# Performance work log

Measured on AMD Instinct MI355X. Metric: run time of the kernel, lower is better.

## Reference

```python
import jax, jax.numpy as jnp
import numpy as np

EMBED = 384
HEADS = 6
HEAD_SIZE = EMBED // HEADS
EPS = 1e-5


def _layernorm(x, g, b):
    mu = jnp.mean(x, axis=-1, keepdims=True)
    var = jnp.mean(jnp.square(x - mu), axis=-1, keepdims=True)
    return (x - mu) * jax.lax.rsqrt(var + EPS) * g + b


def setup_inputs() -> dict:
    key = jax.random.key(0)
    ks = jax.random.split(key, 16)
    B, T = 64, 256
    s_in = 1.0 / np.sqrt(EMBED)
    return {
        "x": jax.random.normal(ks[0], (B, T, EMBED), dtype=jnp.float32),
        # per-head q/k/v projections, stacked over heads: [H, C, D]
        "Wq": jax.random.normal(ks[1], (HEADS, EMBED, HEAD_SIZE), dtype=jnp.float32) * s_in,
        "bq": jnp.zeros((HEADS, HEAD_SIZE), dtype=jnp.float32),
        "Wk": jax.random.normal(ks[2], (HEADS, EMBED, HEAD_SIZE), dtype=jnp.float32) * s_in,
        "bk": jnp.zeros((HEADS, HEAD_SIZE), dtype=jnp.float32),
        "Wv": jax.random.normal(ks[3], (HEADS, EMBED, HEAD_SIZE), dtype=jnp.float32) * s_in,
        "bv": jnp.zeros((HEADS, HEAD_SIZE), dtype=jnp.float32),
        "Wp": jax.random.normal(ks[4], (EMBED, EMBED), dtype=jnp.float32) * s_in,
        "bp": jnp.zeros((EMBED,), dtype=jnp.float32),
        "W1": jax.random.normal(ks[5], (EMBED, EMBED), dtype=jnp.float32) * s_in,
        "b1": jnp.zeros((EMBED,), dtype=jnp.float32),
        "W2": jax.random.normal(ks[6], (EMBED, EMBED), dtype=jnp.float32) * s_in,
        "b2": jnp.zeros((EMBED,), dtype=jnp.float32),
        "ln1_g": jnp.ones((EMBED,), dtype=jnp.float32),
        "ln1_b": jnp.zeros((EMBED,), dtype=jnp.float32),
        "ln2_g": jnp.ones((EMBED,), dtype=jnp.float32),
        "ln2_b": jnp.zeros((EMBED,), dtype=jnp.float32),
    }


def reference(x, Wq, bq, Wk, bk, Wv, bv, Wp, bp, W1, b1, W2, b2,
              ln1_g, ln1_b, ln2_g, ln2_b):
    B, T, C = x.shape
    h = _layernorm(x, ln1_g, ln1_b)
    # batched per-head projections: [B,H,T,D]
    q = jnp.einsum('btc,hcd->bhtd', h, Wq) + bq[None, :, None, :]
    k = jnp.einsum('btc,hcd->bhtd', h, Wk) + bk[None, :, None, :]
    v = jnp.einsum('btc,hcd->bhtd', h, Wv) + bv[None, :, None, :]
    # NOTE: original scales by embed_size**0.5 (C=384), not head_size.
    wei = jnp.einsum('bhtd,bhsd->bhts', q, k) / jnp.sqrt(jnp.float32(C))
    causal = jnp.tril(jnp.ones((T, T), dtype=bool))
    wei = jnp.where(causal[None, None], wei, -jnp.inf)
    wei = jax.nn.softmax(wei, axis=-1)  # dropout = identity in eval
    attn = jnp.einsum('bhts,bhsd->bhtd', wei, v)  # [B,H,T,D]
    # concat heads in head order -> [B,T,C]
    attn = attn.transpose(0, 2, 1, 3).reshape(B, T, C)
    x = x + attn @ Wp + bp
    h2 = _layernorm(x, ln2_g, ln2_b)
    ff = jax.nn.relu(h2 @ W1 + b1) @ W2 + b2
    return x + ff
```

## Files before the change

kernel.cpp:

```cpp
#include <hip/hip_runtime.h>

typedef _Float16 f16;
typedef _Float16 half8 __attribute__((ext_vector_type(8)));
typedef _Float16 half4v __attribute__((ext_vector_type(4)));
typedef float floatx4 __attribute__((ext_vector_type(4)));

#define B_ 64
#define T_ 256
#define C_ 384
#define H_ 6
#define D_ 64
#define NROWS (B_*T_)

typedef __attribute__((address_space(3))) void lds_void_t;
typedef const __attribute__((address_space(1))) void gvoid_t;

__device__ __forceinline__ void g2lds16(const void* g, void* l) {
  __builtin_amdgcn_global_load_lds((gvoid_t*)g, (lds_void_t*)l, 16, 0, 0);
}

__global__ __launch_bounds__(256) void prep_ln_kernel(
    const float* __restrict__ Wq, const float* __restrict__ Wk, const float* __restrict__ Wv,
    const float* __restrict__ bq, const float* __restrict__ bk, const float* __restrict__ bv,
    const float* __restrict__ Wp, const float* __restrict__ W1, const float* __restrict__ W2,
    f16* __restrict__ Wqkv_t, f16* __restrict__ Wp_t, f16* __restrict__ W1_t, f16* __restrict__ W2_t,
    float* __restrict__ bqkv,
    const float* __restrict__ x, const float* __restrict__ gamma, const float* __restrict__ beta,
    f16* __restrict__ hout)
{
  const int bid = blockIdx.x;
  const int tid = threadIdx.x;
  if (bid >= 217) {
    int row = (bid - 217) * 4 + (tid >> 6);
    int lane = tid & 63;
    const float* xr = x + (size_t)row * 384;
    float v[6]; float s = 0.f;
#pragma unroll
    for (int j = 0; j < 6; j++) { v[j] = xr[lane + 64*j]; s += v[j]; }
#pragma unroll
    for (int m = 1; m < 64; m <<= 1) s += __shfl_xor(s, m);
    float mu = s * (1.f/384.f);
    float var = 0.f;
#pragma unroll
    for (int j = 0; j < 6; j++) { float d = v[j]-mu; var += d*d; }
#pragma unroll
    for (int m = 1; m < 64; m <<= 1) var += __shfl_xor(var, m);
    float rs = rsqrtf(var * (1.f/384.f) + 1e-5f);
    f16* orow = hout + (size_t)row*384;
#pragma unroll
    for (int j = 0; j < 6; j++) {
      int col = lane + 64*j;
      orow[col] = (f16)((v[j]-mu)*rs*gamma[col] + beta[col]);
    }
    return;
  }
  if (bid == 216) {
    for (int i = tid; i < 1152; i += 256) {
      float v;
      if (i < 384)      v = bq[i];
      else if (i < 768) v = bk[i - 384];
      else              v = bv[i - 768];
      bqkv[i] = v;
    }
    return;
  }
  __shared__ __align__(16) float tile[64*68];
  const float* src; int srcStride; f16* dst;
  if (bid < 108) {
    int mat = bid / 36, rem = bid - mat*36;
    int h = rem / 6, kt = rem - h*6;
    const float* W = (mat == 0) ? Wq : (mat == 1) ? Wk : Wv;
    src = W + (size_t)(h*384 + kt*64)*64;
    srcStride = 64;
    dst = Wqkv_t + (size_t)(mat*384 + h*64)*384 + kt*64;
  } else {
    int b2 = bid - 108;
    int mat = b2 / 36, rem = b2 - mat*36;
    int kt = rem / 6, ct = rem - kt*6;
    const float* W = (mat == 0) ? Wp : (mat == 1) ? W1 : W2;
    src = W + (size_t)(kt*64)*384 + ct*64;
    srcStride = 384;
    f16* O = (mat == 0) ? Wp_t : (mat == 1) ? W1_t : W2_t;
    dst = O + (size_t)(ct*64)*384 + kt*64;
  }
#pragma unroll
  for (int i = 0; i < 4; i++) {
    int idx = i*256 + tid;
    int r = idx >> 4, c4 = idx & 15;
    float4 v = *(const float4*)(src + (size_t)r*srcStride + c4*4);
    *(float4*)(&tile[r*68 + c4*4]) = v;
  }
  __syncthreads();
#pragma unroll
  for (int i = 0; i < 4; i++) {
    int idx = i*256 + tid;
    int d = idx >> 4, k4 = idx & 15;
    half4v o;
#pragma unroll
    for (int j = 0; j < 4; j++) o[j] = (f16)tile[(k4*4 + j)*68 + d];
    *(half4v*)(dst + (size_t)d*384 + k4*4) = o;
  }
}

__global__ __launch_bounds__(256) void gemm_qkv_kernel(
    const f16* __restrict__ A, const f16* __restrict__ Bt,
    const float* __restrict__ bias, f16* __restrict__ outp, int ldo)
{
  __shared__ __align__(16) f16 As[2][128*32];
  __shared__ __align__(16) f16 Bs[2][128*32];
  const int tid = threadIdx.x;
  const int lane = tid & 63, w = tid >> 6;
  const int wm = w >> 1, wn = w & 1;
  const int q = lane >> 4, c15 = lane & 15;
  const long row0 = (long)blockIdx.x * 128;
  const long col0 = (long)blockIdx.y * 128;
  floatx4 acc[4][4] = {};

  const int c0 = tid,        r0c = c0 >> 2, p0 = c0 & 3, g0 = p0 ^ ((r0c >> 1) & 3);
  const int c1 = 256 + tid,  r1c = c1 >> 2, p1 = c1 & 3, g1 = p1 ^ ((r1c >> 1) & 3);
  const f16* Arow0 = A  + (row0 + r0c)*384 + g0*8;
  const f16* Arow1 = A  + (row0 + r1c)*384 + g1*8;
  const f16* Brow0 = Bt + (col0 + r0c)*384 + g0*8;
  const f16* Brow1 = Bt + (col0 + r1c)*384 + g1*8;
  const int dof0 = (w*64)*8, dof1 = (256 + w*64)*8;

  for (int k0 = 0; k0 < 384; k0 += 64) {
#pragma unroll
    for (int hf = 0; hf < 2; hf++) {
      int kk = k0 + hf*32;
      g2lds16(Arow0 + kk, &As[hf][dof0]);
      g2lds16(Arow1 + kk, &As[hf][dof1]);
      g2lds16(Brow0 + kk, &Bs[hf][dof0]);
      g2lds16(Brow1 + kk, &Bs[hf][dof1]);
    }
    __syncthreads();
#pragma unroll
    for (int hf = 0; hf < 2; hf++) {
      half8 af[4], bf[4];
#pragma unroll
      for (int mi = 0; mi < 4; mi++) {
        int r = wm*64 + mi*16 + c15;
        int ph = q ^ ((r >> 1) & 3);
        af[mi] = *(const half8*)(&As[hf][r*32 + ph*8]);
      }
#pragma unroll
      for (int ni = 0; ni < 4; ni++) {
        int r = wn*64 + ni*16 + c15;
        int ph = q ^ ((r >> 1) & 3);
        bf[ni] = *(const half8*)(&Bs[hf][r*32 + ph*8]);
      }
#pragma unroll
      for (int mi = 0; mi < 4; mi++)
#pragma unroll
        for (int ni = 0; ni < 4; ni++)
          acc[mi][ni] = __builtin_amdgcn_mfma_f32_16x16x32_f16(af[mi], bf[ni], acc[mi][ni], 0, 0, 0);
    }
    __syncthreads();
  }

#pragma unroll
  for (int ni = 0; ni < 4; ni++) {
    long col = col0 + wn*64 + ni*16 + c15;
    float bv = bias[col];
#pragma unroll
    for (int mi = 0; mi < 4; mi++) {
      long rowb = row0 + wm*64 + mi*16 + q*4;
#pragma unroll
      for (int r = 0; r < 4; r++) {
        float vo = acc[mi][ni][r] + bv;
        outp[(rowb + r) * (long)ldo + col] = (f16)vo;
      }
    }
  }
}

__global__ __launch_bounds__(512, 2) void attn_kernel(const f16* __restrict__ qkv,
                                                      f16* __restrict__ attn_out)
{
  __shared__ __align__(16) char kvbuf[32768];
  __shared__ __align__(16) f16 Pbuf[8][16*64];
  f16* Ks = (f16*)kvbuf;
  unsigned int* vTw = (unsigned int*)kvbuf;
  f16* vT = (f16*)kvbuf;

  const int tid = threadIdx.x;
  const int bid = blockIdx.x;
  const int bh = bid >> 1, qt2 = bid & 1;
  const int b = bh / 6, h = bh - b*6;
  const f16* qp = qkv + (size_t)b*256*1152 + h*64;
  const f16* kp = qp + 384;
  const f16* vp = qp + 768;
  const int lane = tid & 63, w = tid >> 6;
  const int q = lane >> 4, c15 = lane & 15;

  {
    const int iters = (qt2 + 1) * 2;
    for (int i = 0; i < iters; i++) {
      int pc = i*512 + tid;
      int rc = pc >> 3, p = pc & 7;
      int c = p ^ (rc & 7);
      g2lds16(kp + (size_t)rc*1152 + c*8, (char*)kvbuf + (size_t)(i*512 + w*64)*16);
    }
  }

  const int nmax = qt2*8 + w;
  const int trow0 = qt2*128 + w*16;
  const f16* qrow = qp + (size_t)(trow0 + c15)*1152 + q*8;
  half8 aq0 = *(const half8*)(qrow);
  half8 aq1 = *(const half8*)(qrow + 32);

  __syncthreads();

  floatx4 sacc[16];
  __builtin_amdgcn_s_setprio(1);
#pragma unroll
  for (int ni = 0; ni < 16; ni++) {
    if (ni <= nmax) {
      int s = ni*16 + c15;
      const f16* kr = Ks + s*64;
      int p0 = q ^ (s & 7);
      half8 b0 = *(const half8*)(kr + p0*8);
      half8 b1 = *(const half8*)(kr + (p0 ^ 4)*8);
      floatx4 a = {0.f, 0.f, 0.f, 0.f};
      a = __builtin_amdgcn_mfma_f32_16x16x32_f16(aq0, b0, a, 0, 0, 0);
      a = __builtin_amdgcn_mfma_f32_16x16x32_f16(aq1, b1, a, 0, 0, 0);
      sacc[ni] = a;
    }
  }
  __builtin_amdgcn_s_setprio(0);
  __syncthreads();

  half8 va[2], vb[2];
#pragma unroll
  for (int i = 0; i < 2; i++) {
    if (i <= qt2) {
      int idx = i*512 + tid;
      int sp = idx >> 3, part = idx & 7;
      const f16* v0 = vp + (size_t)(2*sp)*1152 + part*8;
      va[i] = *(const half8*)(v0);
      vb[i] = *(const half8*)(v0 + 1152);
    }
  }

  const float scale = 0.051031036307982884f;
  float mx[4] = {-1e30f, -1e30f, -1e30f, -1e30f};
#pragma unroll
  for (int ni = 0; ni < 16; ni++) {
    if (ni < nmax) {
#pragma unroll
      for (int r = 0; r < 4; r++) { float v = sacc[ni][r]*scale; sacc[ni][r] = v; mx[r] = fmaxf(mx[r], v); }
    } else if (ni == nmax) {
#pragma unroll
      for (int r = 0; r < 4; r++) {
        float v = sacc[ni][r]*scale;
        v = (c15 <= q*4 + r) ? v : -1e30f;
        sacc[ni][r] = v; mx[r] = fmaxf(mx[r], v);
      }
    }
  }
#pragma unroll
  for (int r = 0; r < 4; r++) {
    mx[r] = fmaxf(mx[r], __shfl_xor(mx[r], 1));
    mx[r] = fmaxf(mx[r], __shfl_xor(mx[r], 2));
    mx[r] = fmaxf(mx[r], __shfl_xor(mx[r], 4));
    mx[r] = fmaxf(mx[r], __shfl_xor(mx[r], 8));
  }
  float l[4] = {0.f, 0.f, 0.f, 0.f};
#pragma unroll
  for (int ni = 0; ni < 16; ni++) {
    if (ni <= nmax) {
#pragma unroll
      for (int r = 0; r < 4; r++) { float p = __expf(sacc[ni][r] - mx[r]); sacc[ni][r] = p; l[r] += p; }
    }
  }
#pragma unroll
  for (int r = 0; r < 4; r++) {
    l[r] += __shfl_xor(l[r], 1);
    l[r] += __shfl_xor(l[r], 2);
    l[r] += __shfl_xor(l[r], 4);
    l[r] += __shfl_xor(l[r], 8);
  }

#pragma unroll
  for (int i = 0; i < 2; i++) {
    if (i <= qt2) {
      int idx = i*512 + tid;
      int sp = idx >> 3, part = idx & 7;
      int csp = sp >> 2, spw = sp & 3;
#pragma unroll
      for (int j = 0; j < 8; j++) {
        int d = part*8 + j;
        int swz = (d & 15) ^ (d >> 3);
        int p = csp ^ swz;
        union { struct { f16 lo, hi; } s; unsigned int u; } pk;
        pk.s.lo = va[i][j]; pk.s.hi = vb[i][j];
        vTw[d*128 + p*4 + spw] = pk.u;
      }
    }
  }
  __syncthreads();

  f16* Pw = &Pbuf[w][0];
  floatx4 oacc[4] = {};
  const int kend_w = (nmax + 1) * 16;
#pragma unroll
  for (int ch = 0; ch < 4; ch++) {
    if (ch*64 < kend_w) {
#pragma unroll
      for (int nl = 0; nl < 4; nl++) {
        int ni = ch*4 + nl;
        if (ni <= nmax) {
#pragma unroll
          for (int r = 0; r < 4; r++) {
            int row = q*4 + r;
            int colp = nl*16 + c15;
            int php = (colp >> 3) ^ (row & 7);
            Pw[row*64 + php*8 + (colp & 7)] = (f16)sacc[ni][r];
          }
        } else if (ni == nmax + 1) {
#pragma unroll
          for (int r = 0; r < 4; r++) {
            int row = q*4 + r;
            int colp = nl*16 + c15;
            int php = (colp >> 3) ^ (row & 7);
            Pw[row*64 + php*8 + (colp & 7)] = (f16)0.f;
          }
        }
      }
      __builtin_amdgcn_s_setprio(1);
#pragma unroll
      for (int kc = 0; kc < 2; kc++) {
        if (ch*64 + kc*32 < kend_w) {
          int pc = (kc*4 + q) ^ (c15 & 7);
          half8 ap = *(const half8*)(Pw + c15*64 + pc*8);
          int sc = ch*8 + kc*4 + q;
#pragma unroll
          for (int nt = 0; nt < 4; nt++) {
            int d = nt*16 + c15;
            int swz = (d & 15) ^ (d >> 3);
            half8 bv = *(const half8*)(vT + d*256 + ((sc ^ swz))*8);
            oacc[nt] = __builtin_amdgcn_mfma_f32_16x16x32_f16(ap, bv, oacc[nt], 0, 0, 0);
          }
        }
      }
      __builtin_amdgcn_s_setprio(0);
    }
  }

  float rl[4];
#pragma unroll
  for (int r = 0; r < 4; r++) rl[r] = 1.0f / l[r];
#pragma unroll
  for (int nt = 0; nt < 4; nt++) {
#pragma unroll
    for (int r = 0; r < 4; r++) {
      int t = trow0 + q*4 + r;
      int d = nt*16 + c15;
      attn_out[(size_t)(b*256 + t)*384 + h*64 + d] = (f16)(oacc[nt][r] * rl[r]);
    }
  }
}

__global__ __launch_bounds__(512, 2) void tail_kernel(
    const f16* __restrict__ A, const f16* __restrict__ WpT,
    const f16* __restrict__ W1T, const f16* __restrict__ W2T,
    const float* __restrict__ bp, const float* __restrict__ b1, const float* __restrict__ b2,
    const float* __restrict__ x, const float* __restrict__ g2, const float* __restrict__ be2,
    float* __restrict__ out)
{
  __shared__ __align__(16) f16 rowbuf[12*64*32];
  __shared__ __align__(16) f16 Bs[2][384*64];
  __shared__ float lnred[2][64][4];
  __shared__ float lnmv[2][64];

  const int tid = threadIdx.x;
  const int lane = tid & 63, w = tid >> 6;
  const int wm = w >> 2, wn = w & 3;
  const int q = lane >> 4, c15 = lane & 15;
  const long row0 = (long)blockIdx.x * 64;

  long offA[6];
#pragma unroll
  for (int i = 0; i < 6; i++) {
    int cb = i*512 + tid;
    int kc = cb >> 8, c2 = cb & 255;
    int rA = c2 >> 2, pA = c2 & 3, gA = pA ^ ((rA >> 1) & 3);
    offA[i] = (row0 + rA)*384 + kc*32 + gA*8;
  }
  long offB[6];
#pragma unroll
  for (int i = 0; i < 6; i++) {
    int cb = i*512 + tid;
    int rc = cb >> 3, r3 = cb & 7;
    int hh = r3 >> 2, p = r3 & 3, g = p ^ ((rc >> 1) & 3);
    offB[i] = (long)rc*384 + hh*32 + g*8;
  }

  floatx4 acc[2][6] = {};

#define T_STAGE_AFULL() do { \
    _Pragma("unroll") \
    for (int i = 0; i < 6; i++) \
      g2lds16(A + offA[i], (char*)rowbuf + (size_t)(i*512 + w*64)*16); \
  } while (0)

#define T_STAGE_B(buf, kk, BT) do { \
    _Pragma("unroll") \
    for (int i = 0; i < 6; i++) \
      g2lds16(BT + offB[i] + (kk), (char*)(&Bs[buf][0]) + (size_t)(i*512 + w*64)*16); \
  } while (0)

#define T_COMP64(a0, buf) do { \
    half8 af[2][2], bf[2][6]; \
    _Pragma("unroll") \
    for (int ks = 0; ks < 2; ks++) { \
      _Pragma("unroll") \
      for (int mi = 0; mi < 2; mi++) { \
        int r = wm*32 + mi*16 + c15; \
        int ph = q ^ ((r >> 1) & 3); \
        af[ks][mi] = *(const half8*)(&rowbuf[((a0) + ks)*2048 + r*32 + ph*8]); \
      } \
      _Pragma("unroll") \
      for (int ni = 0; ni < 6; ni++) { \
        int rb = wn*96 + ni*16 + c15; \
        int phb = q ^ ((rb >> 1) & 3); \
        bf[ks][ni] = *(const half8*)(&Bs[buf][rb*64 + ks*32 + phb*8]); \
      } \
    } \
    _Pragma("unroll") \
    for (int ks = 0; ks < 2; ks++) \
      _Pragma("unroll") \
      for (int mi = 0; mi < 2; mi++) \
        _Pragma("unroll") \
        for (int ni = 0; ni < 6; ni++) \
          acc[mi][ni] = __builtin_amdgcn_mfma_f32_16x16x32_f16(af[ks][mi], bf[ks][ni], acc[mi][ni], 0, 0, 0); \
  } while (0)

  T_STAGE_AFULL();
  T_STAGE_B(0, 0, WpT);
  float xv[2][6][4];
#pragma unroll
  for (int mi = 0; mi < 2; mi++)
#pragma unroll
    for (int rr = 0; rr < 4; rr++) {
      long row = row0 + wm*32 + mi*16 + q*4 + rr;
#pragma unroll
      for (int ni = 0; ni < 6; ni++)
        xv[mi][ni][rr] = x[row*384 + wn*96 + ni*16 + c15];
    }
  __syncthreads();
#pragma unroll
  for (int t = 0; t < 5; ++t) {
    T_STAGE_B((t + 1) & 1, (t + 1) * 64, WpT);
    T_COMP64(2*t, t & 1);
    __syncthreads();
  }
  T_COMP64(10, 1);
  T_STAGE_B(0, 0, W1T);

  float vals[2][6][4];
  {
    float colb[6], cg[6], cb2[6];
#pragma unroll
    for (int ni = 0; ni < 6; ni++) {
      int col = wn*96 + ni*16 + c15;
      colb[ni] = bp[col]; cg[ni] = g2[col]; cb2[ni] = be2[col];
    }
#pragma unroll
    for (int mi = 0; mi < 2; mi++)
#pragma unroll
      for (int rr = 0; rr < 4; rr++)
#pragma unroll
        for (int ni = 0; ni < 6; ni++)
          vals[mi][ni][rr] = acc[mi][ni][rr] + colb[ni] + xv[mi][ni][rr];
#pragma unroll
    for (int mi = 0; mi < 2; mi++) {
#pragma unroll
      for (int rr = 0; rr < 4; rr++) {
        float s = 0.f, s2 = 0.f;
#pragma unroll
        for (int ni = 0; ni < 6; ni++) { float v = vals[mi][ni][rr]; s += v; s2 += v*v; }
        s  += __shfl_xor(s, 1);  s  += __shfl_xor(s, 2);  s  += __shfl_xor(s, 4);  s  += __shfl_xor(s, 8);
        s2 += __shfl_xor(s2, 1); s2 += __shfl_xor(s2, 2); s2 += __shfl_xor(s2, 4); s2 += __shfl_xor(s2, 8);
        if (c15 == 0) {
          int lr = wm*32 + mi*16 + q*4 + rr;
          lnred[0][lr][wn] = s;
          lnred[1][lr][wn] = s2;
        }
      }
    }
    __syncthreads();
    if (tid < 64) {
      float s = 0.f, s2 = 0.f;
#pragma unroll
      for (int j = 0; j < 4; j++) { s += lnred[0][tid][j]; s2 += lnred[1][tid][j]; }
      float mu = s * (1.f/384.f);
      float var = s2 * (1.f/384.f) - mu*mu;
      lnmv[0][tid] = mu;
      lnmv[1][tid] = rsqrtf(var + 1e-5f);
    }
    __syncthreads();
#pragma unroll
    for (int mi = 0; mi < 2; mi++) {
#pragma unroll
      for (int rr = 0; rr < 4; rr++) {
        int lr = wm*32 + mi*16 + q*4 + rr;
        float mu = lnmv[0][lr], rs = lnmv[1][lr];
        int s_ = (lr >> 1) & 3;
#pragma unroll
        for (int ni = 0; ni < 6; ni++) {
          int cc = wn*96 + ni*16 + c15;
          float hv = (vals[mi][ni][rr] - mu)*rs*cg[ni] + cb2[ni];
          int chunk = cc >> 5, kk2 = cc & 31;
          int pos = ((kk2 >> 3) ^ s_)*8 + (kk2 & 7);
          rowbuf[chunk*2048 + lr*32 + pos] = (f16)hv;
        }
      }
    }
  }
  __syncthreads();

#pragma unroll
  for (int mi = 0; mi < 2; mi++)
#pragma unroll
    for (int ni = 0; ni < 6; ni++)
      acc[mi][ni] = floatx4{0.f, 0.f, 0.f, 0.f};
#pragma unroll
  for (int t = 0; t < 5; ++t) {
    T_STAGE_B((t + 1) & 1, (t + 1) * 64, W1T);
    T_COMP64(2*t, t & 1);
    __syncthreads();
  }
  T_COMP64(10, 1);
  T_STAGE_B(0, 0, W2T);
  __syncthreads();

  {
    float colb[6];
#pragma unroll
    for (int ni = 0; ni < 6; ni++) colb[ni] = b1[wn*96 + ni*16 + c15];
#pragma unroll
    for (int mi = 0; mi < 2; mi++) {
#pragma unroll
      for (int rr = 0; rr < 4; rr++) {
        int lr = wm*32 + mi*16 + q*4 + rr;
        int s_ = (lr >> 1) & 3;
#pragma unroll
        for (int ni = 0; ni < 6; ni++) {
          int cc = wn*96 + ni*16 + c15;
          float v = acc[mi][ni][rr] + colb[ni];
          v = v > 0.f ? v : 0.f;
          int chunk = cc >> 5, kk2 = cc & 31;
          int pos = ((kk2 >> 3) ^ s_)*8 + (kk2 & 7);
          rowbuf[chunk*2048 + lr*32 + pos] = (f16)v;
        }
      }
    }
  }
  __syncthreads();

#pragma unroll
  for (int mi = 0; mi < 2; mi++)
#pragma unroll
    for (int ni = 0; ni < 6; ni++)
      acc[mi][ni] = floatx4{0.f, 0.f, 0.f, 0.f};
#pragma unroll
  for (int t = 0; t < 5; ++t) {
    T_STAGE_B((t + 1) & 1, (t + 1) * 64, W2T);
    T_COMP64(2*t, t & 1);
    __syncthreads();
  }
  T_COMP64(10, 1);

  {
    float colb[6];
#pragma unroll
    for (int ni = 0; ni < 6; ni++) colb[ni] = b2[wn*96 + ni*16 + c15];
#pragma unroll
    for (int mi = 0; mi < 2; mi++) {
#pragma unroll
      for (int rr = 0; rr < 4; rr++) {
        long row = row0 + wm*32 + mi*16 + q*4 + rr;
#pragma unroll
        for (int ni = 0; ni < 6; ni++) {
          int col = wn*96 + ni*16 + c15;
          out[row*384 + col] = acc[mi][ni][rr] + colb[ni] + vals[mi][ni][rr];
        }
      }
    }
  }

#undef T_STAGE_AFULL
#undef T_STAGE_B
#undef T_COMP64
}

extern "C" void kernel_launch(void* const* d_in, const int* in_sizes, int n_in,
                              void* d_out, int out_size, void* d_ws, size_t ws_size,
                              hipStream_t stream) {
  const float* x   = (const float*)d_in[0];
  const float* Wq  = (const float*)d_in[1];
  const float* bq  = (const float*)d_in[2];
  const float* Wk  = (const float*)d_in[3];
  const float* bk  = (const float*)d_in[4];
  const float* Wv  = (const float*)d_in[5];
  const float* bv  = (const float*)d_in[6];
  const float* Wp  = (const float*)d_in[7];
  const float* bp  = (const float*)d_in[8];
  const float* W1  = (const float*)d_in[9];
  const float* b1  = (const float*)d_in[10];
  const float* W2  = (const float*)d_in[11];
  const float* b2  = (const float*)d_in[12];
  const float* g1  = (const float*)d_in[13];
  const float* be1 = (const float*)d_in[14];
  const float* g2  = (const float*)d_in[15];
  const float* be2 = (const float*)d_in[16];

  char* ws = (char*)d_ws;
  size_t off = 0;
  auto alloc = [&](size_t bytes) -> void* {
    void* p = ws + off;
    off += (bytes + 255) & ~(size_t)255;
    return p;
  };
  f16*   Wqkv_t = (f16*)  alloc(1152*384*sizeof(f16));
  f16*   Wp_t   = (f16*)  alloc(384*384*sizeof(f16));
  f16*   W1_t   = (f16*)  alloc(384*384*sizeof(f16));
  f16*   W2_t   = (f16*)  alloc(384*384*sizeof(f16));
  float* bqkv   = (float*)alloc(1152*sizeof(float));
  f16*   h      = (f16*)  alloc((size_t)NROWS*384*sizeof(f16));
  f16*   qkv    = (f16*)  alloc((size_t)NROWS*1152*sizeof(f16));
  f16*   attnb  = (f16*)  alloc((size_t)NROWS*384*sizeof(f16));

  prep_ln_kernel<<<217 + NROWS/4, 256, 0, stream>>>(Wq, Wk, Wv, bq, bk, bv, Wp, W1, W2,
                                                    Wqkv_t, Wp_t, W1_t, W2_t, bqkv,
                                                    x, g1, be1, h);
  gemm_qkv_kernel<<<dim3(128, 9), 256, 0, stream>>>(h, Wqkv_t, bqkv, qkv, 1152);
  attn_kernel<<<B_*H_*2, 512, 0, stream>>>(qkv, attnb);
  tail_kernel<<<NROWS/64, 512, 0, stream>>>(attnb, Wp_t, W1_t, W2_t, bp, b1, b2,
                                            x, g2, be2, (float*)d_out);
}
```

Before: 184.1 us.

## Pre-swizzle tail weights into MFMA fragment order and load B directly from global

```diff
diff --git a/kernel.cpp b/kernel.cpp
--- a/kernel.cpp
+++ b/kernel.cpp
@@ -65,7 +65,8 @@
     return;
   }
   __shared__ __align__(16) float tile[64*68];
-  const float* src; int srcStride; f16* dst;
+  const float* src; int srcStride; f16* dst = nullptr;
+  f16* O = nullptr; int kt_ = 0, ct_ = 0; bool frag = false;
   if (bid < 108) {
     int mat = bid / 36, rem = bid - mat*36;
     int h = rem / 6, kt = rem - h*6;
@@ -76,12 +77,12 @@
   } else {
     int b2 = bid - 108;
     int mat = b2 / 36, rem = b2 - mat*36;
-    int kt = rem / 6, ct = rem - kt*6;
+    kt_ = rem / 6; ct_ = rem - kt_*6;
     const float* W = (mat == 0) ? Wp : (mat == 1) ? W1 : W2;
-    src = W + (size_t)(kt*64)*384 + ct*64;
+    src = W + (size_t)(kt_*64)*384 + ct_*64;
     srcStride = 384;
-    f16* O = (mat == 0) ? Wp_t : (mat == 1) ? W1_t : W2_t;
-    dst = O + (size_t)(ct*64)*384 + kt*64;
+    O = (mat == 0) ? Wp_t : (mat == 1) ? W1_t : W2_t;
+    frag = true;
   }
 #pragma unroll
   for (int i = 0; i < 4; i++) {
@@ -98,7 +99,15 @@
     half4v o;
 #pragma unroll
     for (int j = 0; j < 4; j++) o[j] = (f16)tile[(k4*4 + j)*68 + d];
-    *(half4v*)(dst + (size_t)d*384 + k4*4) = o;
+    if (!frag) {
+      *(half4v*)(dst + (size_t)d*384 + k4*4) = o;
+    } else {
+      int ks    = kt_*2 + (k4 >> 3);
+      int ctile = ct_*4 + (d >> 4);
+      int slotq = (k4 >> 1) & 3;
+      size_t off = (size_t)(ks*24 + ctile)*512 + (size_t)(slotq*16 + (d & 15))*8 + (k4 & 1)*4;
+      *(half4v*)(O + off) = o;
+    }
   }
 }
 
@@ -362,14 +371,13 @@
 }
 
 __global__ __launch_bounds__(512, 2) void tail_kernel(
-    const f16* __restrict__ A, const f16* __restrict__ WpT,
-    const f16* __restrict__ W1T, const f16* __restrict__ W2T,
+    const f16* __restrict__ A, const f16* __restrict__ WpR,
+    const f16* __restrict__ W1R, const f16* __restrict__ W2R,
     const float* __restrict__ bp, const float* __restrict__ b1, const float* __restrict__ b2,
     const float* __restrict__ x, const float* __restrict__ g2, const float* __restrict__ be2,
     float* __restrict__ out)
 {
   __shared__ __align__(16) f16 rowbuf[12*64*32];
-  __shared__ __align__(16) f16 Bs[2][384*64];
   __shared__ float lnred[2][64][4];
   __shared__ float lnmv[2][64];
 
@@ -387,57 +395,34 @@
     int rA = c2 >> 2, pA = c2 & 3, gA = pA ^ ((rA >> 1) & 3);
     offA[i] = (row0 + rA)*384 + kc*32 + gA*8;
   }
-  long offB[6];
-#pragma unroll
-  for (int i = 0; i < 6; i++) {
-    int cb = i*512 + tid;
-    int rc = cb >> 3, r3 = cb & 7;
-    int hh = r3 >> 2, p = r3 & 3, g = p ^ ((rc >> 1) & 3);
-    offB[i] = (long)rc*384 + hh*32 + g*8;
-  }
 
   floatx4 acc[2][6] = {};
 
-#define T_STAGE_AFULL() do { \
+#define T_GEMM(WR) do { \
     _Pragma("unroll") \
-    for (int i = 0; i < 6; i++) \
-      g2lds16(A + offA[i], (char*)rowbuf + (size_t)(i*512 + w*64)*16); \
-  } while (0)
-
-#define T_STAGE_B(buf, kk, BT) do { \
-    _Pragma("unroll") \
-    for (int i = 0; i < 6; i++) \
-      g2lds16(BT + offB[i] + (kk), (char*)(&Bs[buf][0]) + (size_t)(i*512 + w*64)*16); \
-  } while (0)
-
-#define T_COMP64(a0, buf) do { \
-    half8 af[2][2], bf[2][6]; \
-    _Pragma("unroll") \
-    for (int ks = 0; ks < 2; ks++) { \
+    for (int kg = 0; kg < 12; kg++) { \
+      half8 af[2]; \
       _Pragma("unroll") \
       for (int mi = 0; mi < 2; mi++) { \
         int r = wm*32 + mi*16 + c15; \
         int ph = q ^ ((r >> 1) & 3); \
-        af[ks][mi] = *(const half8*)(&rowbuf[((a0) + ks)*2048 + r*32 + ph*8]); \
+        af[mi] = *(const half8*)(&rowbuf[kg*2048 + r*32 + ph*8]); \
       } \
+      half8 bf[6]; \
       _Pragma("unroll") \
-      for (int ni = 0; ni < 6; ni++) { \
-        int rb = wn*96 + ni*16 + c15; \
-        int phb = q ^ ((rb >> 1) & 3); \
-        bf[ks][ni] = *(const half8*)(&Bs[buf][rb*64 + ks*32 + phb*8]); \
-      } \
-    } \
-    _Pragma("unroll") \
-    for (int ks = 0; ks < 2; ks++) \
+      for (int ni = 0; ni < 6; ni++) \
+        bf[ni] = *(const half8*)((WR) + (size_t)(kg*24 + wn*6 + ni)*512 + lane*8); \
       _Pragma("unroll") \
       for (int mi = 0; mi < 2; mi++) \
         _Pragma("unroll") \
         for (int ni = 0; ni < 6; ni++) \
-          acc[mi][ni] = __builtin_amdgcn_mfma_f32_16x16x32_f16(af[ks][mi], bf[ks][ni], acc[mi][ni], 0, 0, 0); \
+          acc[mi][ni] = __builtin_amdgcn_mfma_f32_16x16x32_f16(af[mi], bf[ni], acc[mi][ni], 0, 0, 0); \
+    } \
   } while (0)
 
-  T_STAGE_AFULL();
-  T_STAGE_B(0, 0, WpT);
+#pragma unroll
+  for (int i = 0; i < 6; i++)
+    g2lds16(A + offA[i], (char*)rowbuf + (size_t)(i*512 + w*64)*16);
   float xv[2][6][4];
 #pragma unroll
   for (int mi = 0; mi < 2; mi++)
@@ -449,14 +434,8 @@
         xv[mi][ni][rr] = x[row*384 + wn*96 + ni*16 + c15];
     }
   __syncthreads();
-#pragma unroll
-  for (int t = 0; t < 5; ++t) {
-    T_STAGE_B((t + 1) & 1, (t + 1) * 64, WpT);
-    T_COMP64(2*t, t & 1);
-    __syncthreads();
-  }
-  T_COMP64(10, 1);
-  T_STAGE_B(0, 0, W1T);
+
+  T_GEMM(WpR);
 
   float vals[2][6][4];
   {
@@ -525,16 +504,8 @@
 #pragma unroll
     for (int ni = 0; ni < 6; ni++)
       acc[mi][ni] = floatx4{0.f, 0.f, 0.f, 0.f};
-#pragma unroll
-  for (int t = 0; t < 5; ++t) {
-    T_STAGE_B((t + 1) & 1, (t + 1) * 64, W1T);
-    T_COMP64(2*t, t & 1);
-    __syncthreads();
-  }
-  T_COMP64(10, 1);
-  T_STAGE_B(0, 0, W2T);
-  __syncthreads();
-
+  T_GEMM(W1R);
+  __syncthreads();
   {
     float colb[6];
 #pragma unroll
@@ -564,14 +535,7 @@
 #pragma unroll
     for (int ni = 0; ni < 6; ni++)
       acc[mi][ni] = floatx4{0.f, 0.f, 0.f, 0.f};
-#pragma unroll
-  for (int t = 0; t < 5; ++t) {
-    T_STAGE_B((t + 1) & 1, (t + 1) * 64, W2T);
-    T_COMP64(2*t, t & 1);
-    __syncthreads();
-  }
-  T_COMP64(10, 1);
-
+  T_GEMM(W2R);
   {
     float colb[6];
 #pragma unroll
@@ -589,10 +553,7 @@
       }
     }
   }
-
-#undef T_STAGE_AFULL
-#undef T_STAGE_B
-#undef T_COMP64
+#undef T_GEMM
 }
 
 extern "C" void kernel_launch(void* const* d_in, const int* in_sizes, int n_in,
```

New measurement: 181.8 us. Within noise of the previous version (-1.3%).
